# Optimization experiments

Measured on AMD Instinct MI355X. Metric: run time of the kernel, lower is better.

Reference implementation:

```python
import jax, jax.numpy as jnp
import numpy as np

B, H, W, C = 8, 64, 64, 128
BN_EPS = 1e-3  # keras BatchNormalization default epsilon


def setup_inputs() -> dict:
    key = jax.random.key(0)
    ks = jax.random.split(key, 8)
    scale = 1.0 / np.sqrt(C)
    return {
        "x": jax.random.normal(ks[0], (B, H, W, C), dtype=jnp.float32),
        "wq": jax.random.normal(ks[1], (C, C), dtype=jnp.float32) * scale,
        "bq": jnp.zeros((C,), dtype=jnp.float32),
        "wk": jax.random.normal(ks[2], (C, C), dtype=jnp.float32) * scale,
        "bk": jnp.zeros((C,), dtype=jnp.float32),
        "wv": jax.random.normal(ks[3], (C, C), dtype=jnp.float32) * scale,
        "bv": jnp.zeros((C,), dtype=jnp.float32),
        "gamma": jnp.ones((C,), dtype=jnp.float32),
        "beta": jnp.zeros((C,), dtype=jnp.float32),
        "mov_mean": jax.random.normal(ks[4], (C,), dtype=jnp.float32) * 0.1,
        "mov_var": jax.random.uniform(ks[5], (C,), dtype=jnp.float32) * 0.5 + 0.5,
    }


def reference(x, wq, bq, wk, bk, wv, bv, gamma, beta, mov_mean, mov_var):
    b, h, w, c = x.shape
    n = h * w
    # 1x1 convs == per-pixel linear projections
    q = (jnp.einsum('bhwc,cd->bhwd', x, wq) + bq).reshape(b, n, c)
    k = (jnp.einsum('bhwc,cd->bhwd', x, wk) + bk).reshape(b, n, c)
    v = (jnp.einsum('bhwc,cd->bhwd', x, wv) + bv).reshape(b, n, c)
    # full [n, n] attention matrix (as in the original module)
    scores = jnp.einsum('bnc,bmc->bnm', q, k) / jnp.sqrt(jnp.asarray(c, x.dtype))
    attn = jax.nn.softmax(scores, axis=-1)  # dropout is identity in inference
    out = jnp.einsum('bnm,bmc->bnc', attn, v).reshape(b, h, w, c)
    out = out + x  # residual
    # BatchNormalization, inference mode (moving statistics)
    inv = gamma * jax.lax.rsqrt(mov_var + BN_EPS)
    out = out * inv + (beta - mov_mean * inv)
    return out
```

## Files before the change

kernel.cpp:

```cpp
#include <hip/hip_runtime.h>


typedef __attribute__((ext_vector_type(8))) short bf16x8;
typedef __attribute__((ext_vector_type(4))) float f32x4;

__device__ __forceinline__ unsigned short f2bf(float f) {
  unsigned int u = __builtin_bit_cast(unsigned int, f);
  u += 0x7fffu + ((u >> 16) & 1u);
  return (unsigned short)(u >> 16);
}
__device__ __forceinline__ unsigned int pack2(float a, float b) {
  return (unsigned int)f2bf(a) | ((unsigned int)f2bf(b) << 16);
}
__device__ __forceinline__ unsigned int pack2t(float a, float b) {
  return __builtin_amdgcn_perm(__builtin_bit_cast(unsigned int, b),
                               __builtin_bit_cast(unsigned int, a),
                               0x07060302u);
}
__device__ __forceinline__ float fexp2(float x) {
  return __builtin_amdgcn_exp2f(x);
}

__device__ __forceinline__ void dma16(const void* g, void* l) {
  __builtin_amdgcn_global_load_lds(
      (const __attribute__((address_space(1))) unsigned int*)g,
      (__attribute__((address_space(3))) unsigned int*)l, 16, 0, 0);
}

#define SCALE_Q (0.08838834764831845f * 1.44269504088896340f)

__global__ __launch_bounds__(256) void prep_wt(
    const float* __restrict__ wq, const float* __restrict__ wk,
    const float* __restrict__ wv, unsigned short* __restrict__ wt) {
  __shared__ float ws[128 * 129];
  const float* W = (blockIdx.x == 0) ? wq : (blockIdx.x == 1 ? wk : wv);
  const float sc = (blockIdx.x == 0) ? SCALE_Q : 1.0f;
  unsigned short* out = wt + blockIdx.x * 16384;
  const int t = threadIdx.x;

#pragma unroll
  for (int i = 0; i < 16; ++i) {
    int e = (i * 256 + t) * 4;
    float4 v = *(const float4*)(W + e);
    int k = e >> 7, c = e & 127;
    float* d = ws + k * 129 + c;
    d[0] = v.x; d[1] = v.y; d[2] = v.z; d[3] = v.w;
  }
  __syncthreads();

  const int c = t & 15, n0 = t >> 4;
#pragma unroll
  for (int pass = 0; pass < 8; ++pass) {
    int n = pass * 16 + n0;
    const float* col = ws + n;
    unsigned int u0 = pack2(col[(c * 8 + 0) * 129] * sc, col[(c * 8 + 1) * 129] * sc);
    unsigned int u1 = pack2(col[(c * 8 + 2) * 129] * sc, col[(c * 8 + 3) * 129] * sc);
    unsigned int u2 = pack2(col[(c * 8 + 4) * 129] * sc, col[(c * 8 + 5) * 129] * sc);
    unsigned int u3 = pack2(col[(c * 8 + 6) * 129] * sc, col[(c * 8 + 7) * 129] * sc);
    *(uint4*)(out + n * 128 + c * 8) = make_uint4(u0, u1, u2, u3);
  }
}

__global__ __launch_bounds__(256) void qkv_proj(
    const float* __restrict__ x, const unsigned short* __restrict__ wt,
    const float* __restrict__ bq, const float* __restrict__ bk, const float* __restrict__ bv,
    unsigned short* __restrict__ Qg, unsigned short* __restrict__ Kg,
    unsigned short* __restrict__ Vtg) {
  __shared__ unsigned short xs[64 * 128];
  __shared__ unsigned short obuf[9216];
  const int t = threadIdx.x;
  const int rowblk = blockIdx.x * 64;

#pragma unroll
  for (int i = 0; i < 8; ++i) {
    int flat = t * 4 + i * 1024;
    int row = flat >> 7, col = flat & 127;
    float4 v = *(const float4*)(x + (size_t)(rowblk + row) * 128 + col);
    unsigned int u0 = pack2(v.x, v.y), u1 = pack2(v.z, v.w);
    int pos = (col >> 3) ^ (row & 15);
    *(uint2*)(xs + row * 128 + pos * 8 + (col & 7)) = make_uint2(u0, u1);
  }
  __syncthreads();

  const int lane = t & 63, wv_ = t >> 6;
  const int lm = lane & 15, quad = lane >> 4;

  bf16x8 a[4];
  {
    int row = wv_ * 16 + lm;
#pragma unroll
    for (int ks = 0; ks < 4; ++ks)
      a[ks] = __builtin_bit_cast(bf16x8,
          *(const uint4*)(xs + row * 128 + (((ks * 4 + quad) ^ lm) * 8)));
  }

  const int b   = rowblk >> 12;
  const int nb0 = rowblk & 4095;
  const f32x4 zero4 = {0.f, 0.f, 0.f, 0.f};

#pragma unroll
  for (int p = 0; p < 3; ++p) {
    const unsigned short* w = wt + p * 16384;
    const float* bias = (p == 0) ? bq : (p == 1 ? bk : bv);
    const float bsc = (p == 0) ? SCALE_Q : 1.0f;

    f32x4 acc[8];
#pragma unroll
    for (int ct = 0; ct < 8; ++ct) acc[ct] = zero4;

#pragma unroll
    for (int ct = 0; ct < 8; ++ct) {
      int n = ct * 16 + lm;
      const uint4* wp = (const uint4*)(w + n * 128 + quad * 8);
#pragma unroll
      for (int ks = 0; ks < 4; ++ks) {
        bf16x8 bfr = __builtin_bit_cast(bf16x8, wp[ks * 4]);
        acc[ct] = __builtin_amdgcn_mfma_f32_16x16x32_bf16(a[ks], bfr, acc[ct], 0, 0, 0);
      }
    }

    if (p < 2) {
      int rowb = wv_ * 16 + quad * 4;
#pragma unroll
      for (int ct = 0; ct < 8; ++ct) {
        int c = ct * 16 + lm;
        float bb = bias[c] * bsc;
#pragma unroll
        for (int r = 0; r < 4; ++r)
          obuf[(rowb + r) * 136 + c] = f2bf(acc[ct][r] + bb);
      }
      __syncthreads();
      unsigned short* og = (p == 0) ? Qg : Kg;
      int row = t >> 2;
#pragma unroll
      for (int j = 0; j < 4; ++j) {
        int pos = (t & 3) * 4 + j;
        int ch  = (p == 1) ? (pos ^ (row & 15)) : pos;
        uint4 vv = *(const uint4*)(obuf + row * 136 + ch * 8);
        *(uint4*)(og + (size_t)(rowblk + row) * 128 + pos * 8) = vv;
      }
      __syncthreads();
    } else {
      int key_base = wv_ * 16 + quad * 4;
#pragma unroll
      for (int ct = 0; ct < 8; ++ct) {
        int c = ct * 16 + lm;
        float bb = bias[c];
        unsigned int u0 = pack2(acc[ct][0] + bb, acc[ct][1] + bb);
        unsigned int u1 = pack2(acc[ct][2] + bb, acc[ct][3] + bb);
        *(uint2*)(obuf + c * 72 + key_base) = make_uint2(u0, u1);
      }
      __syncthreads();
      int d = t >> 1;
#pragma unroll
      for (int j = 0; j < 4; ++j) {
        int ch = (t & 1) * 4 + j;
        uint4 vv = *(const uint4*)(obuf + d * 72 + ch * 8);
        *(uint4*)(Vtg + (size_t)b * 524288 + (size_t)d * 4096 + nb0 + ch * 8) = vv;
      }
    }
  }
}

__global__ __launch_bounds__(256)
void flash_attn(
    const unsigned short* __restrict__ Qg, const unsigned short* __restrict__ Kg,
    const unsigned short* __restrict__ Vtg, const float* __restrict__ x,
    const float* __restrict__ gamma, const float* __restrict__ beta,
    const float* __restrict__ mmean, const float* __restrict__ mvar,
    float* __restrict__ out) {
  __shared__ unsigned short Kt[8192];
  __shared__ unsigned short Pbuf[2][4096];

  const int b  = blockIdx.x & 7;
  const int qt = blockIdx.x >> 3;
  const int t = threadIdx.x;
  const int lane = t & 63;
  const int w = t >> 6;
  const int lm = lane & 15, quad = lane >> 4;
  const int q0 = qt * 64;

  const unsigned short* Qb = Qg  + (size_t)b * 524288;
  const unsigned short* Kb = Kg  + (size_t)b * 524288;
  const unsigned short* Vb = Vtg + (size_t)b * 524288;

  {
    const unsigned short* src = Kb + (size_t)w * 2048 + lane * 8;
    unsigned short* dst = &Kt[w * 2048];
#pragma unroll
    for (int j = 0; j < 4; ++j) dma16(src + j * 512, dst + j * 512);
  }

  bf16x8 qf[4][4];
#pragma unroll
  for (int nt = 0; nt < 4; ++nt) {
    const uint4* qp = (const uint4*)(Qb + (size_t)(q0 + nt * 16 + lm) * 128 + quad * 8);
#pragma unroll
    for (int ks = 0; ks < 4; ++ks) qf[nt][ks] = __builtin_bit_cast(bf16x8, qp[ks * 4]);
  }

  const f32x4 zero4 = {0.f, 0.f, 0.f, 0.f};
  f32x4 o[2][4];
#pragma unroll
  for (int mt = 0; mt < 2; ++mt)
#pragma unroll
    for (int nt = 0; nt < 4; ++nt) o[mt][nt] = zero4;
  float lp[4] = {0.f, 0.f, 0.f, 0.f};
  bf16x8 vf[2][2];

#pragma unroll 1
  for (int kt = 0; kt < 64; ++kt) {
    const int key0 = kt * 64;

    asm volatile("s_waitcnt vmcnt(4)" ::: "memory");

    f32x4 sa[4];
#pragma unroll
    for (int nt = 0; nt < 4; ++nt) sa[nt] = zero4;
    {
      const unsigned short* kr = &Kt[(w * 16 + lm) * 128];
      bf16x8 kf[4];
#pragma unroll
      for (int ks = 0; ks < 4; ++ks)
        kf[ks] = __builtin_bit_cast(bf16x8, *(const uint4*)(kr + ((ks * 4 + quad) ^ lm) * 8));
#pragma unroll
      for (int ks = 0; ks < 4; ++ks)
#pragma unroll
        for (int nt = 0; nt < 4; ++nt)
          sa[nt] = __builtin_amdgcn_mfma_f32_16x16x32_bf16(kf[ks], qf[nt][ks], sa[nt], 0, 0, 0);
    }

    {
      unsigned short* Ps = Pbuf[kt & 1];
      const int c8 = w * 2 + (quad >> 1);
      const int sub = (quad & 1) * 4;
#pragma unroll
      for (int nt = 0; nt < 4; ++nt) {
        float e0 = fexp2(sa[nt][0]), e1 = fexp2(sa[nt][1]);
        float e2 = fexp2(sa[nt][2]), e3 = fexp2(sa[nt][3]);
        lp[nt] += (e0 + e1) + (e2 + e3);
        int pos = c8 ^ (lm & 7);
        *(uint2*)(Ps + (nt * 16 + lm) * 64 + pos * 8 + sub) =
            make_uint2(pack2t(e0, e1), pack2t(e2, e3));
      }
    }

    asm volatile("s_waitcnt lgkmcnt(0)" ::: "memory");
    if (kt + 1 < 64) {
      const unsigned short* src = Kb + (size_t)(kt + 1) * 8192 + w * 2048 + lane * 8;
      unsigned short* dst = &Kt[w * 2048];
#pragma unroll
      for (int j = 0; j < 4; ++j) dma16(src + j * 512, dst + j * 512);
    }

    if (kt > 0) {
      const uint4* Pr = (const uint4*)Pbuf[(kt & 1) ^ 1];
#pragma unroll
      for (int nt = 0; nt < 4; ++nt) {
        bf16x8 pf[2];
#pragma unroll
        for (int ks = 0; ks < 2; ++ks)
          pf[ks] = __builtin_bit_cast(bf16x8, Pr[(nt * 16 + lm) * 8 + ((ks * 4 + quad) ^ (lm & 7))]);
#pragma unroll
        for (int ks = 0; ks < 2; ++ks)
#pragma unroll
          for (int mt = 0; mt < 2; ++mt)
            o[mt][nt] = __builtin_amdgcn_mfma_f32_16x16x32_bf16(vf[mt][ks], pf[ks], o[mt][nt], 0, 0, 0);
      }
    }

#pragma unroll
    for (int mt = 0; mt < 2; ++mt) {
      const uint4* vp = (const uint4*)(Vb + (size_t)(w * 32 + mt * 16 + lm) * 4096 + key0 + quad * 8);
#pragma unroll
      for (int ks = 0; ks < 2; ++ks) vf[mt][ks] = __builtin_bit_cast(bf16x8, vp[ks * 4]);
    }

    asm volatile("s_waitcnt lgkmcnt(0)\n\ts_barrier" ::: "memory");
  }

  {
    const uint4* Pr = (const uint4*)Pbuf[1];
#pragma unroll
    for (int nt = 0; nt < 4; ++nt) {
      bf16x8 pf[2];
#pragma unroll
      for (int ks = 0; ks < 2; ++ks)
        pf[ks] = __builtin_bit_cast(bf16x8, Pr[(nt * 16 + lm) * 8 + ((ks * 4 + quad) ^ (lm & 7))]);
#pragma unroll
      for (int ks = 0; ks < 2; ++ks)
#pragma unroll
        for (int mt = 0; mt < 2; ++mt)
          o[mt][nt] = __builtin_amdgcn_mfma_f32_16x16x32_bf16(vf[mt][ks], pf[ks], o[mt][nt], 0, 0, 0);
    }
  }

  float* lred = (float*)Pbuf[0];
#pragma unroll
  for (int nt = 0; nt < 4; ++nt) {
    lp[nt] += __shfl_xor(lp[nt], 16);
    lp[nt] += __shfl_xor(lp[nt], 32);
  }
  if (quad == 0) {
#pragma unroll
    for (int nt = 0; nt < 4; ++nt) lred[w * 64 + nt * 16 + lm] = lp[nt];
  }
  __syncthreads();
  float rl[4];
#pragma unroll
  for (int nt = 0; nt < 4; ++nt) {
    int q = nt * 16 + lm;
    rl[nt] = 1.0f / ((lred[q] + lred[64 + q]) + (lred[128 + q] + lred[192 + q]));
  }

#pragma unroll
  for (int mt = 0; mt < 2; ++mt) {
    int c0 = w * 32 + mt * 16 + quad * 4;
    float4 gm = *(const float4*)(gamma + c0);
    float4 bt = *(const float4*)(beta + c0);
    float4 mm = *(const float4*)(mmean + c0);
    float4 mv = *(const float4*)(mvar + c0);
    float iv0 = gm.x * rsqrtf(mv.x + 1e-3f), iv1 = gm.y * rsqrtf(mv.y + 1e-3f);
    float iv2 = gm.z * rsqrtf(mv.z + 1e-3f), iv3 = gm.w * rsqrtf(mv.w + 1e-3f);
    float ad0 = bt.x - mm.x * iv0, ad1 = bt.y - mm.y * iv1;
    float ad2 = bt.z - mm.z * iv2, ad3 = bt.w - mm.w * iv3;
#pragma unroll
    for (int nt = 0; nt < 4; ++nt) {
      size_t g = ((size_t)b * 4096 + q0 + nt * 16 + lm) * 128 + c0;
      float4 xr = *(const float4*)(x + g);
      float4 ov;
      ov.x = (o[mt][nt][0] * rl[nt] + xr.x) * iv0 + ad0;
      ov.y = (o[mt][nt][1] * rl[nt] + xr.y) * iv1 + ad1;
      ov.z = (o[mt][nt][2] * rl[nt] + xr.z) * iv2 + ad2;
      ov.w = (o[mt][nt][3] * rl[nt] + xr.w) * iv3 + ad3;
      *(float4*)(out + g) = ov;
    }
  }
}

extern "C" void kernel_launch(void* const* d_in, const int* in_sizes, int n_in,
                              void* d_out, int out_size, void* d_ws, size_t ws_size,
                              hipStream_t stream) {
  const float* x     = (const float*)d_in[0];
  const float* wq    = (const float*)d_in[1];
  const float* bq    = (const float*)d_in[2];
  const float* wk    = (const float*)d_in[3];
  const float* bk    = (const float*)d_in[4];
  const float* wv    = (const float*)d_in[5];
  const float* bv    = (const float*)d_in[6];
  const float* gamma = (const float*)d_in[7];
  const float* beta  = (const float*)d_in[8];
  const float* mmean = (const float*)d_in[9];
  const float* mvar  = (const float*)d_in[10];
  float* out = (float*)d_out;

  unsigned short* wt  = (unsigned short*)d_ws;
  unsigned short* Qg  = wt + 3 * 128 * 128;
  unsigned short* Kg  = Qg + 8 * 4096 * 128;
  unsigned short* Vtg = Kg + 8 * 4096 * 128;

  prep_wt<<<dim3(3), dim3(256), 0, stream>>>(wq, wk, wv, wt);
  qkv_proj<<<dim3(512), dim3(256), 0, stream>>>(x, wt, bq, bk, bv, Qg, Kg, Vtg);
  flash_attn<<<dim3(512), dim3(256), 0, stream>>>(Qg, Kg, Vtg, x, gamma, beta,
                                                  mmean, mvar, out);
}
```

Measured before the change: 207.3 us.

## Use 8 waves per flash-attention block with 128-key tiles

```diff
diff --git a/kernel.cpp b/kernel.cpp
--- a/kernel.cpp
+++ b/kernel.cpp
@@ -162,15 +162,15 @@
   }
 }
 
-__global__ __launch_bounds__(256)
+__global__ __launch_bounds__(512)
 void flash_attn(
     const unsigned short* __restrict__ Qg, const unsigned short* __restrict__ Kg,
     const unsigned short* __restrict__ Vtg, const float* __restrict__ x,
     const float* __restrict__ gamma, const float* __restrict__ beta,
     const float* __restrict__ mmean, const float* __restrict__ mvar,
     float* __restrict__ out) {
-  __shared__ unsigned short Kt[8192];
-  __shared__ unsigned short Pbuf[2][4096];
+  __shared__ unsigned short Kt[16384];
+  __shared__ unsigned short Pbuf[2][8192];
 
   const int b  = blockIdx.x & 7;
   const int qt = blockIdx.x >> 3;
@@ -200,17 +200,15 @@
   }
 
   const f32x4 zero4 = {0.f, 0.f, 0.f, 0.f};
-  f32x4 o[2][4];
-#pragma unroll
-  for (int mt = 0; mt < 2; ++mt)
-#pragma unroll
-    for (int nt = 0; nt < 4; ++nt) o[mt][nt] = zero4;
+  f32x4 o[4];
+#pragma unroll
+  for (int nt = 0; nt < 4; ++nt) o[nt] = zero4;
   float lp[4] = {0.f, 0.f, 0.f, 0.f};
-  bf16x8 vf[2][2];
+  bf16x8 vf[4];
 
 #pragma unroll 1
-  for (int kt = 0; kt < 64; ++kt) {
-    const int key0 = kt * 64;
+  for (int kt = 0; kt < 32; ++kt) {
+    const int key0 = kt * 128;
 
     asm volatile("s_waitcnt vmcnt(4)" ::: "memory");
 
@@ -232,22 +230,22 @@
 
     {
       unsigned short* Ps = Pbuf[kt & 1];
-      const int c8 = w * 2 + (quad >> 1);
+      const int c16 = w * 2 + (quad >> 1);
       const int sub = (quad & 1) * 4;
 #pragma unroll
       for (int nt = 0; nt < 4; ++nt) {
         float e0 = fexp2(sa[nt][0]), e1 = fexp2(sa[nt][1]);
         float e2 = fexp2(sa[nt][2]), e3 = fexp2(sa[nt][3]);
         lp[nt] += (e0 + e1) + (e2 + e3);
-        int pos = c8 ^ (lm & 7);
-        *(uint2*)(Ps + (nt * 16 + lm) * 64 + pos * 8 + sub) =
+        int pos = c16 ^ lm;
+        *(uint2*)(Ps + (nt * 16 + lm) * 128 + pos * 8 + sub) =
             make_uint2(pack2t(e0, e1), pack2t(e2, e3));
       }
     }
 
     asm volatile("s_waitcnt lgkmcnt(0)" ::: "memory");
-    if (kt + 1 < 64) {
-      const unsigned short* src = Kb + (size_t)(kt + 1) * 8192 + w * 2048 + lane * 8;
+    if (kt + 1 < 32) {
+      const unsigned short* src = Kb + (size_t)(kt + 1) * 16384 + w * 2048 + lane * 8;
       unsigned short* dst = &Kt[w * 2048];
 #pragma unroll
       for (int j = 0; j < 4; ++j) dma16(src + j * 512, dst + j * 512);
@@ -257,23 +255,20 @@
       const uint4* Pr = (const uint4*)Pbuf[(kt & 1) ^ 1];
 #pragma unroll
       for (int nt = 0; nt < 4; ++nt) {
-        bf16x8 pf[2];
-#pragma unroll
-        for (int ks = 0; ks < 2; ++ks)
-          pf[ks] = __builtin_bit_cast(bf16x8, Pr[(nt * 16 + lm) * 8 + ((ks * 4 + quad) ^ (lm & 7))]);
-#pragma unroll
-        for (int ks = 0; ks < 2; ++ks)
-#pragma unroll
-          for (int mt = 0; mt < 2; ++mt)
-            o[mt][nt] = __builtin_amdgcn_mfma_f32_16x16x32_bf16(vf[mt][ks], pf[ks], o[mt][nt], 0, 0, 0);
-      }
-    }
-
-#pragma unroll
-    for (int mt = 0; mt < 2; ++mt) {
-      const uint4* vp = (const uint4*)(Vb + (size_t)(w * 32 + mt * 16 + lm) * 4096 + key0 + quad * 8);
-#pragma unroll
-      for (int ks = 0; ks < 2; ++ks) vf[mt][ks] = __builtin_bit_cast(bf16x8, vp[ks * 4]);
+        bf16x8 pf[4];
+#pragma unroll
+        for (int ks = 0; ks < 4; ++ks)
+          pf[ks] = __builtin_bit_cast(bf16x8, Pr[(nt * 16 + lm) * 16 + ((ks * 4 + quad) ^ lm)]);
+#pragma unroll
+        for (int ks = 0; ks < 4; ++ks)
+          o[nt] = __builtin_amdgcn_mfma_f32_16x16x32_bf16(vf[ks], pf[ks], o[nt], 0, 0, 0);
+      }
+    }
+
+    {
+      const uint4* vp = (const uint4*)(Vb + (size_t)(w * 16 + lm) * 4096 + key0 + quad * 8);
+#pragma unroll
+      for (int ks = 0; ks < 4; ++ks) vf[ks] = __builtin_bit_cast(bf16x8, vp[ks * 4]);
     }
 
     asm volatile("s_waitcnt lgkmcnt(0)\n\ts_barrier" ::: "memory");
@@ -283,15 +278,13 @@
     const uint4* Pr = (const uint4*)Pbuf[1];
 #pragma unroll
     for (int nt = 0; nt < 4; ++nt) {
-      bf16x8 pf[2];
-#pragma unroll
-      for (int ks = 0; ks < 2; ++ks)
-        pf[ks] = __builtin_bit_cast(bf16x8, Pr[(nt * 16 + lm) * 8 + ((ks * 4 + quad) ^ (lm & 7))]);
-#pragma unroll
-      for (int ks = 0; ks < 2; ++ks)
-#pragma unroll
-        for (int mt = 0; mt < 2; ++mt)
-          o[mt][nt] = __builtin_amdgcn_mfma_f32_16x16x32_bf16(vf[mt][ks], pf[ks], o[mt][nt], 0, 0, 0);
+      bf16x8 pf[4];
+#pragma unroll
+      for (int ks = 0; ks < 4; ++ks)
+        pf[ks] = __builtin_bit_cast(bf16x8, Pr[(nt * 16 + lm) * 16 + ((ks * 4 + quad) ^ lm)]);
+#pragma unroll
+      for (int ks = 0; ks < 4; ++ks)
+        o[nt] = __builtin_amdgcn_mfma_f32_16x16x32_bf16(vf[ks], pf[ks], o[nt], 0, 0, 0);
     }
   }
 
@@ -310,12 +303,13 @@
 #pragma unroll
   for (int nt = 0; nt < 4; ++nt) {
     int q = nt * 16 + lm;
-    rl[nt] = 1.0f / ((lred[q] + lred[64 + q]) + (lred[128 + q] + lred[192 + q]));
-  }
-
-#pragma unroll
-  for (int mt = 0; mt < 2; ++mt) {
-    int c0 = w * 32 + mt * 16 + quad * 4;
+    float s0 = (lred[q] + lred[64 + q]) + (lred[128 + q] + lred[192 + q]);
+    float s1 = (lred[256 + q] + lred[320 + q]) + (lred[384 + q] + lred[448 + q]);
+    rl[nt] = 1.0f / (s0 + s1);
+  }
+
+  {
+    int c0 = w * 16 + quad * 4;
     float4 gm = *(const float4*)(gamma + c0);
     float4 bt = *(const float4*)(beta + c0);
     float4 mm = *(const float4*)(mmean + c0);
@@ -329,10 +323,10 @@
       size_t g = ((size_t)b * 4096 + q0 + nt * 16 + lm) * 128 + c0;
       float4 xr = *(const float4*)(x + g);
       float4 ov;
-      ov.x = (o[mt][nt][0] * rl[nt] + xr.x) * iv0 + ad0;
-      ov.y = (o[mt][nt][1] * rl[nt] + xr.y) * iv1 + ad1;
-      ov.z = (o[mt][nt][2] * rl[nt] + xr.z) * iv2 + ad2;
-      ov.w = (o[mt][nt][3] * rl[nt] + xr.w) * iv3 + ad3;
+      ov.x = (o[nt][0] * rl[nt] + xr.x) * iv0 + ad0;
+      ov.y = (o[nt][1] * rl[nt] + xr.y) * iv1 + ad1;
+      ov.z = (o[nt][2] * rl[nt] + xr.z) * iv2 + ad2;
+      ov.w = (o[nt][3] * rl[nt] + xr.w) * iv3 + ad3;
       *(float4*)(out + g) = ov;
     }
   }
@@ -361,6 +355,6 @@
 
   prep_wt<<<dim3(3), dim3(256), 0, stream>>>(wq, wk, wv, wt);
   qkv_proj<<<dim3(512), dim3(256), 0, stream>>>(x, wt, bq, bk, bv, Qg, Kg, Vtg);
-  flash_attn<<<dim3(512), dim3(256), 0, stream>>>(Qg, Kg, Vtg, x, gamma, beta,
+  flash_attn<<<dim3(512), dim3(512), 0, stream>>>(Qg, Kg, Vtg, x, gamma, beta,
                                                   mmean, mvar, out);
 }
```

Measured after the change: 218.7 us. 1.05x slower.
